# Kernel tuning notes

Hardware: AMD Instinct MI355X
Metric: run time of the kernel (lower is better)

The kernel has to match this reference:

```python
import jax, jax.numpy as jnp
import numpy as np

N, IN_DIM, OUT_DIM = 8192, 256, 128
NEG_BIG = -9e15


def setup_inputs() -> dict:
    key = jax.random.key(0)
    k_x, k_a, k_w, k_att = jax.random.split(key, 4)
    X = jax.random.normal(k_x, (N, IN_DIM), dtype=jnp.float32)
    A = jax.random.randint(k_a, (N, N), 0, 2).astype(jnp.float32)
    # nn.Linear(in_dim, out_dim, bias=False): weight [out_dim, in_dim]
    W = jax.random.normal(k_w, (OUT_DIM, IN_DIM), dtype=jnp.float32) / np.sqrt(IN_DIM)
    # nn.Linear(out_dim, 1, bias=False): weight [1, out_dim] -> store as [out_dim]
    a_w = jax.random.normal(k_att, (OUT_DIM,), dtype=jnp.float32) / np.sqrt(OUT_DIM)
    return {"X": X, "A": A, "W": W, "a_w": a_w}


def reference(X, A, W, a_w):
    Wh = X @ W.T                                  # [N, out_dim]
    e = jax.nn.relu(Wh) @ a_w                      # [N]  (a(relu(Wh)).squeeze(-1))
    # NOTE: faithful to source: e broadcasts over rows -> score[i, j] = e[j]
    scores = jnp.where(A > 0, e[None, :], NEG_BIG)  # [N, N]
    attention = jax.nn.softmax(scores, axis=1)      # [N, N]
    h_prime = attention @ Wh                        # [N, out_dim]
    return jax.nn.relu(h_prime)
```

## Files before the change

### kernel.cpp

```cpp
#include <hip/hip_runtime.h>

typedef float        f32x4  __attribute__((ext_vector_type(4)));
typedef __bf16       bf16x8 __attribute__((ext_vector_type(8)));
typedef unsigned int u32x4  __attribute__((ext_vector_type(4)));

#define NN   8192
#define IND  256
#define OUTD 128
#define NB   144
#define KSPLIT 8
#define KRANGE 1024
#define KCHUNK 128
#define BSTRIDE 136

__device__ __forceinline__ bf16x8 cvt2(f32x4 a, f32x4 b) {
  bf16x8 r;
  r[0]=(__bf16)a[0]; r[1]=(__bf16)a[1]; r[2]=(__bf16)a[2]; r[3]=(__bf16)a[3];
  r[4]=(__bf16)b[0]; r[5]=(__bf16)b[1]; r[6]=(__bf16)b[2]; r[7]=(__bf16)b[3];
  return r;
}

__global__ __launch_bounds__(256) void k1_bt(const float* __restrict__ X,
                                             const float* __restrict__ W,
                                             const float* __restrict__ aw,
                                             __bf16* __restrict__ Bt) {
  __shared__ float red[4][16][128];
  const int tid  = threadIdx.x;
  const int lane = tid & 63;
  const int wave = tid >> 6;
  const int nlo  = lane & 15;
  const int quad = lane >> 4;
  const int rowBase = blockIdx.x * 16;

  const float* xp = X + (size_t)(rowBase + nlo) * IND + wave * 64 + quad * 8;
  f32x4 acc[8];
#pragma unroll
  for (int nt = 0; nt < 8; ++nt) acc[nt] = f32x4{0.f, 0.f, 0.f, 0.f};

#pragma unroll
  for (int kb = 0; kb < 64; kb += 32) {
    f32x4 a0 = *(const f32x4*)(xp + kb);
    f32x4 a1 = *(const f32x4*)(xp + kb + 4);
    bf16x8 af = cvt2(a0, a1);
#pragma unroll
    for (int nt = 0; nt < 8; ++nt) {
      const float* wp = W + (size_t)(nt * 16 + nlo) * IND + wave * 64 + kb + quad * 8;
      f32x4 b0 = *(const f32x4*)wp;
      f32x4 b1 = *(const f32x4*)(wp + 4);
      acc[nt] = __builtin_amdgcn_mfma_f32_16x16x32_bf16(af, cvt2(b0, b1), acc[nt], 0, 0, 0);
    }
  }
#pragma unroll
  for (int nt = 0; nt < 8; ++nt)
#pragma unroll
    for (int rg = 0; rg < 4; ++rg)
      red[wave][quad * 4 + rg][nt * 16 + nlo] = acc[nt][rg];
  __syncthreads();

  const int r  = tid >> 4;
  const int c0 = (tid & 15) * 8;
  f32x4 vlo = *(const f32x4*)&red[0][r][c0];
  f32x4 vhi = *(const f32x4*)&red[0][r][c0 + 4];
#pragma unroll
  for (int w = 1; w < 4; ++w) {
    vlo += *(const f32x4*)&red[w][r][c0];
    vhi += *(const f32x4*)&red[w][r][c0 + 4];
  }
  float pa = 0.f;
#pragma unroll
  for (int i = 0; i < 4; ++i) {
    pa += fmaxf(vlo[i], 0.f) * aw[c0 + i];
    pa += fmaxf(vhi[i], 0.f) * aw[c0 + 4 + i];
  }
#pragma unroll
  for (int off = 8; off; off >>= 1) pa += __shfl_xor(pa, off, 64);
  const float wexp = expf(pa);
  const int j = rowBase + r;

#pragma unroll
  for (int i = 0; i < 4; ++i)
    Bt[(size_t)(c0 + i) * NN + j] = (__bf16)(vlo[i] * wexp);
#pragma unroll
  for (int i = 0; i < 4; ++i)
    Bt[(size_t)(c0 + 4 + i) * NN + j] = (__bf16)(vhi[i] * wexp);
  if ((tid & 15) == 0)
    Bt[(size_t)OUTD * NN + j] = (__bf16)wexp;
  if (tid < 120) {
    const int row = 129 + (tid >> 3);
    const int cc  = rowBase + (tid & 7) * 2;
    Bt[(size_t)row * NN + cc]     = (__bf16)0.f;
    Bt[(size_t)row * NN + cc + 1] = (__bf16)0.f;
  }
}

__global__ __launch_bounds__(256, 4) void k3_partial(const float* __restrict__ Adj,
                                                     const __bf16* __restrict__ Bt,
                                                     float* __restrict__ part) {
  __shared__ unsigned short bt[NB * BSTRIDE];
  const int tid  = threadIdx.x;
  const int lane = tid & 63;
  const int wave = tid >> 6;
  const int nlo  = lane & 15;
  const int quad = lane >> 4;
  const int rowW = blockIdx.x * 64 + wave * 16;
  const int k0   = blockIdx.y * KRANGE;

  const int brow = tid >> 4;
  const int bcol = (tid & 15) * 8;

  f32x4 acc[9];
#pragma unroll
  for (int nt = 0; nt < 9; ++nt) acc[nt] = f32x4{0.f, 0.f, 0.f, 0.f};

  const float* ap = Adj + (size_t)(rowW + nlo) * NN + quad * 8 + k0;

  for (int c = 0; c < KRANGE / KCHUNK; ++c) {
    const int kc = k0 + c * KCHUNK;
    u32x4 breg[9];
#pragma unroll
    for (int rr = 0; rr < 9; ++rr)
      breg[rr] = *(const u32x4*)(Bt + (size_t)(rr * 16 + brow) * NN + kc + bcol);
    f32x4 areg[8];
#pragma unroll
    for (int s = 0; s < 4; ++s) {
      areg[2 * s]     = __builtin_nontemporal_load((const f32x4*)(ap + c * KCHUNK + s * 32));
      areg[2 * s + 1] = __builtin_nontemporal_load((const f32x4*)(ap + c * KCHUNK + s * 32 + 4));
    }
#pragma unroll
    for (int rr = 0; rr < 9; ++rr)
      *(u32x4*)(bt + (rr * 16 + brow) * BSTRIDE + bcol) = breg[rr];
    __syncthreads();
#pragma unroll
    for (int s = 0; s < 4; ++s) {
      bf16x8 af = cvt2(areg[2 * s], areg[2 * s + 1]);
      const unsigned short* bp = bt + s * 32 + quad * 8;
#pragma unroll
      for (int nt = 0; nt < 9; ++nt) {
        bf16x8 bf = *(const bf16x8*)(bp + (nt * 16 + nlo) * BSTRIDE);
        acc[nt] = __builtin_amdgcn_mfma_f32_16x16x32_bf16(af, bf, acc[nt], 0, 0, 0);
      }
    }
    __syncthreads();
  }

  float* pbase = part + ((size_t)blockIdx.y * NN + rowW) * NB;
#pragma unroll
  for (int nt = 0; nt < 8; ++nt)
#pragma unroll
    for (int rg = 0; rg < 4; ++rg)
      pbase[(size_t)(quad * 4 + rg) * NB + nt * 16 + nlo] = acc[nt][rg];
  if (nlo == 0) {
#pragma unroll
    for (int rg = 0; rg < 4; ++rg)
      pbase[(size_t)(quad * 4 + rg) * NB + 128] = acc[8][rg];
  }
}

__global__ __launch_bounds__(256) void k3_reduce(const float* __restrict__ part,
                                                 float* __restrict__ out) {
  const int col = threadIdx.x & 127;
  const int row = blockIdx.x * 2 + (threadIdx.x >> 7);
  float num = 0.f, den = 0.f;
#pragma unroll
  for (int s = 0; s < KSPLIT; ++s) {
    const size_t base = ((size_t)s * NN + row) * NB;
    num += part[base + col];
    den += part[base + 128];
  }
  out[(size_t)row * OUTD + col] = fmaxf(num / den, 0.f);
}

extern "C" void kernel_launch(void* const* d_in, const int* in_sizes, int n_in,
                              void* d_out, int out_size, void* d_ws, size_t ws_size,
                              hipStream_t stream) {
  const float* X  = (const float*)d_in[0];
  const float* A  = (const float*)d_in[1];
  const float* W  = (const float*)d_in[2];
  const float* aw = (const float*)d_in[3];
  float* out = (float*)d_out;

  char* ws = (char*)d_ws;
  __bf16* Bt   = (__bf16*)ws;
  float*  part = (float*)(ws + 4194304);

  k1_bt<<<512, 256, 0, stream>>>(X, W, aw, Bt);
  k3_partial<<<dim3(128, KSPLIT), 256, 0, stream>>>(A, Bt, part);
  k3_reduce<<<4096, 256, 0, stream>>>(part, out);
}
```

Baseline: 403.4 us.

## Stage adjacency tile through LDS with coalesced loads and double rows per block

Measured after the change: 400.1 us, median of 2. No clear change (-0.8%).

```diff
diff --git a/kernel.cpp b/kernel.cpp
--- a/kernel.cpp
+++ b/kernel.cpp
@@ -11,7 +11,8 @@
 #define KSPLIT 8
 #define KRANGE 1024
 #define KCHUNK 128
-#define BSTRIDE 136
+#define ASTR 136
+#define BSTR 136
 
 __device__ __forceinline__ bf16x8 cvt2(f32x4 a, f32x4 b) {
   bf16x8 r;
@@ -93,50 +94,59 @@
   }
 }
 
-__global__ __launch_bounds__(256, 4) void k3_partial(const float* __restrict__ Adj,
+__global__ __launch_bounds__(512, 4) void k3_partial(const float* __restrict__ Adj,
                                                      const __bf16* __restrict__ Bt,
                                                      float* __restrict__ part) {
-  __shared__ unsigned short bt[NB * BSTRIDE];
+  __shared__ unsigned short aT[128 * ASTR];
+  __shared__ unsigned short bT[NB * BSTR];
   const int tid  = threadIdx.x;
   const int lane = tid & 63;
-  const int wave = tid >> 6;
+  const int wv   = tid >> 6;
   const int nlo  = lane & 15;
   const int quad = lane >> 4;
-  const int rowW = blockIdx.x * 64 + wave * 16;
+  const int rowW = blockIdx.x * 128 + wv * 16;
   const int k0   = blockIdx.y * KRANGE;
 
-  const int brow = tid >> 4;
-  const int bcol = (tid & 15) * 8;
+  const int lrow = tid >> 4;
+  const int lcol = (tid & 15) * 8;
+
+  const float*  aload = Adj + (size_t)((size_t)blockIdx.x * 128 + lrow) * NN + k0 + lcol;
+  const __bf16* bload = Bt + (size_t)lrow * NN + k0 + lcol;
 
   f32x4 acc[9];
 #pragma unroll
   for (int nt = 0; nt < 9; ++nt) acc[nt] = f32x4{0.f, 0.f, 0.f, 0.f};
 
-  const float* ap = Adj + (size_t)(rowW + nlo) * NN + quad * 8 + k0;
-
   for (int c = 0; c < KRANGE / KCHUNK; ++c) {
-    const int kc = k0 + c * KCHUNK;
-    u32x4 breg[9];
+    const int kc = c * KCHUNK;
+    u32x4 breg[5];
 #pragma unroll
-    for (int rr = 0; rr < 9; ++rr)
-      breg[rr] = *(const u32x4*)(Bt + (size_t)(rr * 16 + brow) * NN + kc + bcol);
+    for (int r = 0; r < 4; ++r)
+      breg[r] = *(const u32x4*)(bload + (size_t)(r * 32) * NN + kc);
+    if (lrow < 16)
+      breg[4] = *(const u32x4*)(bload + (size_t)128 * NN + kc);
     f32x4 areg[8];
 #pragma unroll
-    for (int s = 0; s < 4; ++s) {
-      areg[2 * s]     = __builtin_nontemporal_load((const f32x4*)(ap + c * KCHUNK + s * 32));
-      areg[2 * s + 1] = __builtin_nontemporal_load((const f32x4*)(ap + c * KCHUNK + s * 32 + 4));
+    for (int r = 0; r < 4; ++r) {
+      areg[2 * r]     = __builtin_nontemporal_load((const f32x4*)(aload + (size_t)(r * 32) * NN + kc));
+      areg[2 * r + 1] = __builtin_nontemporal_load((const f32x4*)(aload + (size_t)(r * 32) * NN + kc + 4));
     }
 #pragma unroll
-    for (int rr = 0; rr < 9; ++rr)
-      *(u32x4*)(bt + (rr * 16 + brow) * BSTRIDE + bcol) = breg[rr];
+    for (int r = 0; r < 4; ++r)
+      *(u32x4*)(bT + (r * 32 + lrow) * BSTR + lcol) = breg[r];
+    if (lrow < 16)
+      *(u32x4*)(bT + (128 + lrow) * BSTR + lcol) = breg[4];
+#pragma unroll
+    for (int r = 0; r < 4; ++r)
+      *(bf16x8*)(aT + (r * 32 + lrow) * ASTR + lcol) = cvt2(areg[2 * r], areg[2 * r + 1]);
     __syncthreads();
+
 #pragma unroll
     for (int s = 0; s < 4; ++s) {
-      bf16x8 af = cvt2(areg[2 * s], areg[2 * s + 1]);
-      const unsigned short* bp = bt + s * 32 + quad * 8;
+      bf16x8 af = *(const bf16x8*)(aT + (wv * 16 + nlo) * ASTR + s * 32 + quad * 8);
 #pragma unroll
       for (int nt = 0; nt < 9; ++nt) {
-        bf16x8 bf = *(const bf16x8*)(bp + (nt * 16 + nlo) * BSTRIDE);
+        bf16x8 bf = *(const bf16x8*)(bT + (nt * 16 + nlo) * BSTR + s * 32 + quad * 8);
         acc[nt] = __builtin_amdgcn_mfma_f32_16x16x32_bf16(af, bf, acc[nt], 0, 0, 0);
       }
     }
@@ -184,6 +194,6 @@
   float*  part = (float*)(ws + 4194304);
 
   k1_bt<<<512, 256, 0, stream>>>(X, W, aw, Bt);
-  k3_partial<<<dim3(128, KSPLIT), 256, 0, stream>>>(A, Bt, part);
+  k3_partial<<<dim3(64, KSPLIT), 512, 0, stream>>>(A, Bt, part);
   k3_reduce<<<4096, 256, 0, stream>>>(part, out);
 }
```

## Fuse split-K partial and reduce into single full-K kernel with 32-row tiles

Applied to the files above, without the earlier changes.

After: 448.0 us. +11.0%, slower.

```diff
diff --git a/kernel.cpp b/kernel.cpp
--- a/kernel.cpp
+++ b/kernel.cpp
@@ -2,16 +2,15 @@
 
 typedef float        f32x4  __attribute__((ext_vector_type(4)));
 typedef __bf16       bf16x8 __attribute__((ext_vector_type(8)));
+typedef __bf16       bf16x4 __attribute__((ext_vector_type(4)));
 typedef unsigned int u32x4  __attribute__((ext_vector_type(4)));
 
 #define NN   8192
 #define IND  256
 #define OUTD 128
-#define NB   144
-#define KSPLIT 8
-#define KRANGE 1024
 #define KCHUNK 128
-#define BSTRIDE 136
+#define ASTR 136
+#define BSTR 136
 
 __device__ __forceinline__ bf16x8 cvt2(f32x4 a, f32x4 b) {
   bf16x8 r;
@@ -93,81 +92,84 @@
   }
 }
 
-__global__ __launch_bounds__(256, 4) void k3_partial(const float* __restrict__ Adj,
-                                                     const __bf16* __restrict__ Bt,
-                                                     float* __restrict__ part) {
-  __shared__ unsigned short bt[NB * BSTRIDE];
+__global__ __launch_bounds__(256) void k3_fused(const float* __restrict__ Adj,
+                                                const __bf16* __restrict__ Bt,
+                                                float* __restrict__ out) {
+  __shared__ unsigned short aT[32 * ASTR];
+  __shared__ unsigned short bT[144 * BSTR];
+  __shared__ float dend[32];
   const int tid  = threadIdx.x;
   const int lane = tid & 63;
-  const int wave = tid >> 6;
+  const int wv   = tid >> 6;
   const int nlo  = lane & 15;
   const int quad = lane >> 4;
-  const int rowW = blockIdx.x * 64 + wave * 16;
-  const int k0   = blockIdx.y * KRANGE;
+  const int rowgrp = wv & 1;
+  const int ntgrp  = wv >> 1;
+  const int nt0 = ntgrp ? 5 : 0;
+  const int ntn = ntgrp ? 4 : 5;
+  const int rowBase = blockIdx.x * 32;
 
+  const int arow = tid >> 3;
+  const int acol = (tid & 7) * 16;
   const int brow = tid >> 4;
   const int bcol = (tid & 15) * 8;
 
-  f32x4 acc[9];
+  const float*  aload = Adj + (size_t)(rowBase + arow) * NN + acol;
+  const __bf16* bload = Bt + (size_t)brow * NN + bcol;
+
+  f32x4 acc[5];
 #pragma unroll
-  for (int nt = 0; nt < 9; ++nt) acc[nt] = f32x4{0.f, 0.f, 0.f, 0.f};
+  for (int t = 0; t < 5; ++t) acc[t] = f32x4{0.f, 0.f, 0.f, 0.f};
 
-  const float* ap = Adj + (size_t)(rowW + nlo) * NN + quad * 8 + k0;
-
-  for (int c = 0; c < KRANGE / KCHUNK; ++c) {
-    const int kc = k0 + c * KCHUNK;
+  for (int c = 0; c < NN / KCHUNK; ++c) {
+    const int kc = c * KCHUNK;
     u32x4 breg[9];
 #pragma unroll
     for (int rr = 0; rr < 9; ++rr)
-      breg[rr] = *(const u32x4*)(Bt + (size_t)(rr * 16 + brow) * NN + kc + bcol);
-    f32x4 areg[8];
+      breg[rr] = *(const u32x4*)(bload + (size_t)(rr * 16) * NN + kc);
+    f32x4 areg[4];
+#pragma unroll
+    for (int j = 0; j < 4; ++j)
+      areg[j] = __builtin_nontemporal_load((const f32x4*)(aload + kc + j * 4));
+#pragma unroll
+    for (int rr = 0; rr < 9; ++rr)
+      *(u32x4*)(bT + (rr * 16 + brow) * BSTR + bcol) = breg[rr];
+    *(bf16x8*)(aT + arow * ASTR + acol)     = cvt2(areg[0], areg[1]);
+    *(bf16x8*)(aT + arow * ASTR + acol + 8) = cvt2(areg[2], areg[3]);
+    __syncthreads();
+
 #pragma unroll
     for (int s = 0; s < 4; ++s) {
-      areg[2 * s]     = __builtin_nontemporal_load((const f32x4*)(ap + c * KCHUNK + s * 32));
-      areg[2 * s + 1] = __builtin_nontemporal_load((const f32x4*)(ap + c * KCHUNK + s * 32 + 4));
-    }
+      bf16x8 af = *(const bf16x8*)(aT + (rowgrp * 16 + nlo) * ASTR + s * 32 + quad * 8);
 #pragma unroll
-    for (int rr = 0; rr < 9; ++rr)
-      *(u32x4*)(bt + (rr * 16 + brow) * BSTRIDE + bcol) = breg[rr];
-    __syncthreads();
-#pragma unroll
-    for (int s = 0; s < 4; ++s) {
-      bf16x8 af = cvt2(areg[2 * s], areg[2 * s + 1]);
-      const unsigned short* bp = bt + s * 32 + quad * 8;
-#pragma unroll
-      for (int nt = 0; nt < 9; ++nt) {
-        bf16x8 bf = *(const bf16x8*)(bp + (nt * 16 + nlo) * BSTRIDE);
-        acc[nt] = __builtin_amdgcn_mfma_f32_16x16x32_bf16(af, bf, acc[nt], 0, 0, 0);
+      for (int t = 0; t < 5; ++t) {
+        if (t < ntn) {
+          bf16x8 bf = *(const bf16x8*)(bT + ((nt0 + t) * 16 + nlo) * BSTR + s * 32 + quad * 8);
+          acc[t] = __builtin_amdgcn_mfma_f32_16x16x32_bf16(af, bf, acc[t], 0, 0, 0);
+        }
       }
     }
     __syncthreads();
   }
 
-  float* pbase = part + ((size_t)blockIdx.y * NN + rowW) * NB;
-#pragma unroll
-  for (int nt = 0; nt < 8; ++nt)
+  if (ntgrp == 1 && nlo == 0) {
 #pragma unroll
     for (int rg = 0; rg < 4; ++rg)
-      pbase[(size_t)(quad * 4 + rg) * NB + nt * 16 + nlo] = acc[nt][rg];
-  if (nlo == 0) {
+      dend[rowgrp * 16 + quad * 4 + rg] = acc[3][rg];
+  }
+  __syncthreads();
+
+  const int nstore = ntgrp ? 3 : 5;
 #pragma unroll
-    for (int rg = 0; rg < 4; ++rg)
-      pbase[(size_t)(quad * 4 + rg) * NB + 128] = acc[8][rg];
+  for (int rg = 0; rg < 4; ++rg) {
+    const float den = dend[rowgrp * 16 + quad * 4 + rg];
+    const int row = rowBase + rowgrp * 16 + quad * 4 + rg;
+#pragma unroll
+    for (int t = 0; t < 5; ++t) {
+      if (t < nstore)
+        out[(size_t)row * OUTD + (nt0 + t) * 16 + nlo] = fmaxf(acc[t][rg] / den, 0.f);
+    }
   }
-}
-
-__global__ __launch_bounds__(256) void k3_reduce(const float* __restrict__ part,
-                                                 float* __restrict__ out) {
-  const int col = threadIdx.x & 127;
-  const int row = blockIdx.x * 2 + (threadIdx.x >> 7);
-  float num = 0.f, den = 0.f;
-#pragma unroll
-  for (int s = 0; s < KSPLIT; ++s) {
-    const size_t base = ((size_t)s * NN + row) * NB;
-    num += part[base + col];
-    den += part[base + 128];
-  }
-  out[(size_t)row * OUTD + col] = fmaxf(num / den, 0.f);
 }
 
 extern "C" void kernel_launch(void* const* d_in, const int* in_sizes, int n_in,
@@ -179,11 +181,8 @@
   const float* aw = (const float*)d_in[3];
   float* out = (float*)d_out;
 
-  char* ws = (char*)d_ws;
-  __bf16* Bt   = (__bf16*)ws;
-  float*  part = (float*)(ws + 4194304);
+  __bf16* Bt = (__bf16*)d_ws;
 
   k1_bt<<<512, 256, 0, stream>>>(X, W, aw, Bt);
-  k3_partial<<<dim3(128, KSPLIT), 256, 0, stream>>>(A, Bt, part);
-  k3_reduce<<<4096, 256, 0, stream>>>(part, out);
+  k3_fused<<<256, 256, 0, stream>>>(A, Bt, out);
 }
```
